# Kernel optimization log

Hardware: AMD Instinct MI355X
Metric: run time of the kernel (lower is better)

## Reference

```python
import jax, jax.numpy as jnp
import numpy as np

# dims
T, B, N, H = 16, 8, 8, 128            # time, batch, num_schemas, schema_dim
C, IH, IW = 32, 16, 16                # conv_dims
TASK, ACT, REW = 128, 16, 1
HEADS = 7
TAR = TASK + ACT + REW                # 145
CTX = H + TAR                         # 273 context_dim
CONV_FLAT = C * IH * IW               # 8192
MEM_IN = CONV_FLAT + H + CTX          # 8593


def setup_inputs() -> dict:
    key = jax.random.key(0)
    ks = jax.random.split(key, 20)
    def n(k, shape, s=0.02):
        return jax.random.normal(k, shape, dtype=jnp.float32) * s
    D = HEADS * H
    return {
        "image": jax.random.normal(ks[0], (T, B, C, IH, IW), dtype=jnp.float32),
        "task_action_reward": jax.random.normal(ks[1], (T, B, TAR), dtype=jnp.float32),
        # MultiHeadedAttention params
        "Wq_w": n(ks[2], (D, CTX)), "Wq_b": jnp.zeros((D,), jnp.float32),
        "Wk_w": n(ks[3], (D, H)),   "Wk_b": jnp.zeros((D,), jnp.float32),
        "Wv_w": n(ks[4], (D, H)),   "Wv_b": jnp.zeros((D,), jnp.float32),
        "Wo_w": n(ks[5], (H, D)),   "Wo_b": jnp.zeros((H,), jnp.float32),
        # TopdownFeatureAttention: N per-query linears (stacked) + 1x1 conv
        "td_w": n(ks[6], (N, C, CTX)), "td_b": jnp.zeros((N, C), jnp.float32),
        "conv_w": n(ks[7], (C, C)), "conv_b": jnp.zeros((C,), jnp.float32),
        # ListStructuredRnn: N per-schema LSTM cells (PyTorch gate order i,f,g,o)
        "Wih": n(ks[8], (N, 4 * H, MEM_IN)), "Whh": n(ks[9], (N, 4 * H, H)),
        "bih": jnp.zeros((N, 4 * H), jnp.float32), "bhh": jnp.zeros((N, 4 * H), jnp.float32),
    }


def reference(image, task_action_reward, Wq_w, Wq_b, Wk_w, Wk_b, Wv_w, Wv_b,
              Wo_w, Wo_b, td_w, td_b, conv_w, conv_b, Wih, Whh, bih, bhh):
    f32 = image.dtype
    # prev_state=None path: prev_h is zeros for all timesteps
    prev_h = jnp.zeros((T, B, N, H), f32)
    # schema_context = duplicate task_action_reward over schemas, cat prev_h -> (T,B,N,CTX)
    ctx = jnp.concatenate(
        [jnp.broadcast_to(task_action_reward[:, :, None, :], (T, B, N, TAR)), prev_h], axis=-1)
    # keys = cat(prev_h, zeros) along schema axis -> (T,B,N+1,H)
    keys = jnp.concatenate([prev_h, jnp.zeros((T, B, 1, H), f32)], axis=2)

    # --- MultiHeadedAttention (no mask; dropout unused in forward) ---
    q = (ctx @ Wq_w.T + Wq_b).reshape(T, B, N, HEADS, H)
    k = (keys @ Wk_w.T + Wk_b).reshape(T, B, N + 1, HEADS, H)
    v = (keys @ Wv_w.T + Wv_b).reshape(T, B, N + 1, HEADS, H)
    scores = jnp.einsum('tbqhd,tbkhd->tbhqk', q, k) / jnp.sqrt(jnp.asarray(H, f32))
    attn = jax.nn.softmax(scores, axis=-1)
    xatt = jnp.einsum('tbhqk,tbkhd->tbqhd', attn, v).reshape(T, B, N, HEADS * H)
    shared = xatt @ Wo_w.T + Wo_b                      # (T,B,N,H)

    # --- TopdownFeatureAttention: per-query linear -> sigmoid channel gate -> 1x1 conv ---
    gate = jax.nn.sigmoid(jnp.einsum('tbnx,ncx->tbnc', ctx, td_w) + td_b)   # (T,B,N,C)
    modulated = image[:, :, None] * gate[..., None, None]                    # (T,B,N,C,IH,IW)
    conv = jnp.einsum('tbnchw,dc->tbndhw', modulated, conv_w) + conv_b[:, None, None]
    schema_updates = conv.reshape(T, B, N, CONV_FLAT)

    # --- per-schema LSTMs over time (zero initial state) ---
    mem = jnp.concatenate([schema_updates, shared, ctx], axis=-1)            # (T,B,N,MEM_IN)
    xg = jnp.einsum('tbni,ngi->tbng', mem, Wih) + bih + bhh                  # (T,B,N,4H)

    def step(carry, g_t):
        h, c = carry
        g = g_t + jnp.einsum('bnh,ngh->bng', h, Whh)
        i, f, gg, o = jnp.split(g, 4, axis=-1)
        c = jax.nn.sigmoid(f) * c + jax.nn.sigmoid(i) * jnp.tanh(gg)
        h = jax.nn.sigmoid(o) * jnp.tanh(c)
        return (h, c), h

    z = jnp.zeros((B, N, H), f32)
    (hT, cT), hs = jax.lax.scan(step, (z, z), xg)
    outs = hs.reshape(T, B, N * H)
    return outs, hT, cT
```

## Files before the change

kernel.cpp:

```cpp
#include <hip/hip_runtime.h>

#define T_   16
#define B_   8
#define N_   8
#define H_   128
#define C_   32
#define HW_  256
#define TAR_ 145
#define G4H  512
#define MEMIN 8593
#define AK   8512
#define XGN  524288
#define KSTEP 64

typedef __attribute__((ext_vector_type(8))) short short8v;
typedef __attribute__((ext_vector_type(4))) float f32x4;
typedef __attribute__((ext_vector_type(4), aligned(4))) float f32x4u;

__device__ __forceinline__ float bf2f(unsigned short u){
  return __uint_as_float(((unsigned int)u) << 16);
}
__device__ __forceinline__ unsigned short f2bf(float x){
  unsigned int b = __float_as_uint(x);
  return (unsigned short)((b + 0x7fffu + ((b >> 16) & 1u)) >> 16);
}
__device__ __forceinline__ unsigned pkbf(float lo, float hi){
  return __builtin_amdgcn_perm(__float_as_uint(hi) + 0x8000u,
                               __float_as_uint(lo) + 0x8000u, 0x07060302u);
}
__device__ __forceinline__ float bflo(unsigned w){ return __uint_as_float(w << 16); }
__device__ __forceinline__ float bfhi(unsigned w){ return __uint_as_float(w & 0xffff0000u); }
__device__ __forceinline__ float sigf(float x){ return 1.f/(1.f + expf(-x)); }

__device__ __forceinline__ void gl_lds16(const void* g, void* l){
  __builtin_amdgcn_global_load_lds(
      (const __attribute__((address_space(1))) unsigned int*)g,
      (__attribute__((address_space(3))) unsigned int*)l, 16, 0, 0);
}
__device__ __forceinline__ void gl_lds4(const void* g, void* l){
  __builtin_amdgcn_global_load_lds(
      (const __attribute__((address_space(1))) unsigned int*)g,
      (__attribute__((address_space(3))) unsigned int*)l, 4, 0, 0);
}

__global__ void k_shared(const float* __restrict__ WvB, const float* __restrict__ WoW,
                         const float* __restrict__ WoB, float* __restrict__ sh){
  const int h = blockIdx.x, lane = threadIdx.x;
  float acc = 0.f;
  for(int d = lane; d < 896; d += 64) acc += WvB[d] * WoW[h*896 + d];
  for(int s = 32; s; s >>= 1) acc += __shfl_down(acc, s);
  if(lane == 0) sh[h] = acc + WoB[h];
}

__global__ __launch_bounds__(256) void k_gate(const float* __restrict__ tar,
                                              const float* __restrict__ tdw,
                                              const float* __restrict__ tdb,
                                              float* __restrict__ gate){
  __shared__ float twS[32*145];
  __shared__ float taS[16*145];
  const int tb0 = blockIdx.x * 16, n = blockIdx.y, tid = threadIdx.x;
  for(int i = tid; i < 32*145; i += 256){
    int c = i / 145, x = i - c*145;
    twS[i] = tdw[(n*32 + c)*273 + x];
  }
  for(int i = tid; i < 16*145; i += 256)
    taS[i] = tar[tb0*145 + i];
  __syncthreads();
  for(int o = tid; o < 512; o += 256){
    int r = o >> 5, c = o & 31;
    float a = tdb[n*32 + c];
    const float* tr = &taS[r*145];
    const float* tw = &twS[c*145];
    for(int x = 0; x < 145; ++x) a += tr[x]*tw[x];
    gate[((tb0 + r)*N_ + n)*C_ + c] = 1.f/(1.f + expf(-a));
  }
}

__global__ __launch_bounds__(256) void k_conv2(
    const float* __restrict__ img, const float* __restrict__ gate,
    const float* __restrict__ cw, const float* __restrict__ cb,
    const float* __restrict__ sh, const float* __restrict__ tar,
    unsigned short* __restrict__ mem)
{
  __shared__ float imgS[8192];
  __shared__ float cwgT[1024];
  const int tb = blockIdx.x, n = blockIdx.y;
  const int hw = threadIdx.x;
  for(int i = hw; i < 8192; i += 256)
    imgS[i] = img[(size_t)tb*8192 + i];
  for(int i = hw; i < 1024; i += 256){
    const int c = i >> 5, d = i & 31;
    cwgT[i] = cw[d*32 + c] * gate[(tb*8 + n)*32 + c];
  }
  __syncthreads();
  f32x4 acc[8];
  #pragma unroll
  for(int dq = 0; dq < 8; ++dq){
    const f32x4u cv = *(const f32x4u*)&cb[dq*4];
    acc[dq].x = cv.x; acc[dq].y = cv.y; acc[dq].z = cv.z; acc[dq].w = cv.w;
  }
  #pragma unroll 4
  for(int c = 0; c < 32; ++c){
    const float iv = imgS[c*256 + hw];
    #pragma unroll
    for(int dq = 0; dq < 8; ++dq){
      const f32x4 w = *(const f32x4*)&cwgT[c*32 + dq*4];
      acc[dq].x += iv*w.x; acc[dq].y += iv*w.y;
      acc[dq].z += iv*w.z; acc[dq].w += iv*w.w;
    }
  }
  unsigned short* mrow = mem + (size_t)(n*128 + tb)*AK;
  #pragma unroll
  for(int dq = 0; dq < 8; ++dq){
    mrow[(dq*4 + 0)*256 + hw] = f2bf(acc[dq].x);
    mrow[(dq*4 + 1)*256 + hw] = f2bf(acc[dq].y);
    mrow[(dq*4 + 2)*256 + hw] = f2bf(acc[dq].z);
    mrow[(dq*4 + 3)*256 + hw] = f2bf(acc[dq].w);
  }
  for(int i = hw; i < 320; i += 256){
    if(i < 128)      mrow[8192 + i]       = f2bf(sh[i]);
    else if(i < 273) mrow[8320 + i - 128] = f2bf(tar[tb*TAR_ + i - 128]);
    else             mrow[8465 + i - 273] = 0;
  }
}

__global__ __launch_bounds__(256) void k_gemm5(
    const unsigned short* __restrict__ mem, const float* __restrict__ Wih,
    float* __restrict__ xg4)
{
  __shared__ unsigned short Abuf[2][128*64];
  __shared__ float          Bbuf[2][16*64];
  const int gt = blockIdx.x, n = blockIdx.y, ks = blockIdx.z;
  const int tid = threadIdx.x;
  const int wv = tid >> 6, ln = tid & 63;
  const int lr = ln & 15, lg = ln >> 4;
  const int g0 = gt*16;
  const int kbeg = (ks == 0) ? 0 : 2176 + (ks - 1)*2112;
  const int nsteps = (ks == 0) ? 34 : 33;
  const unsigned short* An = mem + (size_t)n*128*AK;
  const float* Bn = Wih + (size_t)(n*G4H + g0)*MEMIN;

#define STAGE5(bb, kk) do{                                                     \
    _Pragma("unroll")                                                          \
    for(int i_ = 0; i_ < 4; ++i_){                                             \
      const int ci_ = i_*256 + tid;                                            \
      const int row_ = ci_ >> 3;                                               \
      const unsigned short* src_ = An + (size_t)row_*AK + (kk)                 \
                                   + (((ci_ & 7) ^ (row_ & 7)) << 3);          \
      gl_lds16(src_, &Abuf[bb][(i_*256 + wv*64)*8]);                           \
    }                                                                          \
    _Pragma("unroll")                                                          \
    for(int q_ = 0; q_ < 4; ++q_){                                             \
      const int idx_ = q_*256 + tid;                                           \
      const int g_ = idx_ >> 6;                                                \
      const int kd_ = idx_ & 63;                                               \
      const float* srcB_ = Bn + (size_t)g_*MEMIN + (kk)                        \
                           + ((((kd_ >> 3) ^ (g_ & 7)) << 3) + (kd_ & 7));     \
      gl_lds4(srcB_, &Bbuf[bb][q_*256 + wv*64]);                               \
    }                                                                          \
  }while(0)

  f32x4 acc0 = {0.f,0.f,0.f,0.f};
  f32x4 acc1 = {0.f,0.f,0.f,0.f};

  STAGE5(0, kbeg);
  if(nsteps > 1) STAGE5(1, kbeg + KSTEP);

  int b = 0;
  for(int t = 0; t < nsteps; ++t){
    if(t < nsteps - 1){
      asm volatile("s_waitcnt vmcnt(8)" ::: "memory");
    } else {
      asm volatile("s_waitcnt vmcnt(0)" ::: "memory");
    }
    __builtin_amdgcn_s_barrier();
    #pragma unroll
    for(int s = 0; s < 2; ++s){
      const int jb = (s*4 + lg) ^ (lr & 7);
      const float* bp = &Bbuf[b][lr*64 + jb*8];
      const f32x4 blo = *(const f32x4*)bp;
      const f32x4 bhi = *(const f32x4*)(bp + 4);
      short8v bf;
      unsigned* u = (unsigned*)&bf;
      u[0] = pkbf(blo.x, blo.y); u[1] = pkbf(blo.z, blo.w);
      u[2] = pkbf(bhi.x, bhi.y); u[3] = pkbf(bhi.z, bhi.w);
      const short8v a0 = *(const short8v*)&Abuf[b][(wv*32 + lr)*64 + jb*8];
      const short8v a1 = *(const short8v*)&Abuf[b][(wv*32 + 16 + lr)*64 + jb*8];
      acc0 = __builtin_amdgcn_mfma_f32_16x16x32_bf16(a0, bf, acc0, 0, 0, 0);
      acc1 = __builtin_amdgcn_mfma_f32_16x16x32_bf16(a1, bf, acc1, 0, 0, 0);
    }
    __builtin_amdgcn_s_barrier();
    if(t + 2 < nsteps) STAGE5(b, kbeg + (t+2)*KSTEP);
    b ^= 1;
  }
#undef STAGE5

  float* dst = xg4 + (size_t)ks*XGN;
  const int c0 = g0 + lr;
  const int r0 = wv*32 + lg*4, r1 = r0 + 16;
  #pragma unroll
  for(int j = 0; j < 4; ++j){
    dst[(size_t)((r0 + j)*8 + n)*G4H + c0] = acc0[j];
    dst[(size_t)((r1 + j)*8 + n)*G4H + c0] = acc1[j];
  }
}

__global__ __launch_bounds__(512) void k_lstm2(
    const float* __restrict__ xg4, const float* __restrict__ Whh,
    const float* __restrict__ bih, const float* __restrict__ bhh,
    float* __restrict__ out)
{
  __shared__ float hS[128];
  __shared__ float preS[512];
  const int bn = blockIdx.x;
  const int n = bn & 7, b = bn >> 3;
  const int g = threadIdx.x;

  unsigned wr[64];
  const float* wrow = Whh + (size_t)(n*G4H + g)*H_;
  #pragma unroll
  for(int i = 0; i < 32; ++i){
    const f32x4 w = *(const f32x4*)(wrow + i*4);
    wr[2*i]   = pkbf(w.x, w.y);
    wr[2*i+1] = pkbf(w.z, w.w);
  }
  const float bias = bih[n*G4H + g] + bhh[n*G4H + g];
  if(g < 128) hS[g] = 0.f;
  float cc = 0.f;
  __syncthreads();

  for(int t = 0; t < 16; ++t){
    const size_t xb = (size_t)((t*8 + b)*8 + n)*G4H + g;
    float acc = bias + xg4[xb] + xg4[xb + XGN] + xg4[xb + 2*XGN] + xg4[xb + 3*XGN];
    #pragma unroll
    for(int q = 0; q < 32; ++q){
      const f32x4 hv = *(const f32x4*)&hS[q*4];
      const unsigned w0 = wr[2*q], w1 = wr[2*q+1];
      acc += hv.x*bflo(w0) + hv.y*bfhi(w0) + hv.z*bflo(w1) + hv.w*bfhi(w1);
    }
    preS[g] = acc;
    __syncthreads();
    if(g < 128){
      const float iv = sigf(preS[g]);
      const float fv = sigf(preS[128 + g]);
      const float gv = tanhf(preS[256 + g]);
      const float ov = sigf(preS[384 + g]);
      cc = fv*cc + iv*gv;
      const float hn = ov*tanhf(cc);
      hS[g] = hn;
      out[(t*8 + b)*1024 + n*128 + g] = hn;
      if(t == 15){
        out[131072 + (b*8 + n)*128 + g] = hn;
        out[139264 + (b*8 + n)*128 + g] = cc;
      }
    }
    __syncthreads();
  }
}

__global__ __launch_bounds__(512) void k_conv(
    const float* __restrict__ img, const float* __restrict__ gate,
    const float* __restrict__ cw, const float* __restrict__ cb,
    const float* __restrict__ sh, const float* __restrict__ tar,
    unsigned short* __restrict__ mem)
{
  __shared__ float imgS[8192];
  __shared__ float cwgS[1024];
  __shared__ float shS[128];
  __shared__ float tarS[160];
  const int tb = blockIdx.x, tid = threadIdx.x;
  for(int i = tid; i < 8192; i += 512)
    imgS[i] = img[(size_t)tb*8192 + i];
  if(tid < 128) shS[tid] = sh[tid];
  if(tid >= 128 && tid < 273) tarS[tid-128] = tar[tb*TAR_ + tid - 128];
  for(int n = 0; n < 8; ++n){
    __syncthreads();
    for(int i = tid; i < 1024; i += 512)
      cwgS[i] = cw[i] * gate[(tb*8 + n)*32 + (i & 31)];
    __syncthreads();
    unsigned short* mrow = mem + (size_t)(n*128 + tb)*AK;
    for(int q = 0; q < 4; ++q){
      const int idx = q*2048 + tid*4;
      const int d = idx >> 8, hw = idx & 255;
      const float bias = cb[d];
      float a0 = bias, a1 = bias, a2 = bias, a3 = bias;
      const float* cg = &cwgS[d*32];
      #pragma unroll
      for(int c = 0; c < 32; ++c){
        const f32x4 iv = *(const f32x4*)&imgS[c*256 + hw];
        const float w = cg[c];
        a0 += w*iv.x; a1 += w*iv.y; a2 += w*iv.z; a3 += w*iv.w;
      }
      ushort4 o;
      o.x = f2bf(a0); o.y = f2bf(a1); o.z = f2bf(a2); o.w = f2bf(a3);
      *(ushort4*)&mrow[idx] = o;
    }
    if(tid < 128)      mrow[8192 + tid]       = f2bf(shS[tid]);
    else if(tid < 273) mrow[8320 + tid - 128] = f2bf(tarS[tid - 128]);
    else if(tid < 320) mrow[8465 + tid - 273] = 0;
  }
}

__global__ __launch_bounds__(256) void k_bias(const float* __restrict__ bih,
                                              const float* __restrict__ bhh,
                                              float* __restrict__ xg){
  const int i = blockIdx.x*256 + threadIdx.x;
  const int ng = ((i >> 9) & 7)*512 + (i & 511);
  xg[i] = bih[ng] + bhh[ng];
}

__global__ __launch_bounds__(256) void k_gemm_mfma(
    const unsigned short* __restrict__ mem, const float* __restrict__ Wih,
    float* __restrict__ xg)
{
  const int gt = blockIdx.x, n = blockIdx.y, ks = blockIdx.z;
  const int wv = threadIdx.x >> 6, ln = threadIdx.x & 63;
  const int lr = ln & 15, lg = ln >> 4;
  const int g0 = gt*16;
  const int kbeg = (ks==0) ? 0 : (ks==1) ? 2144 : (ks==2) ? 4256 : 6368;
  const int kend = (ks==0) ? 2144 : (ks==1) ? 4256 : (ks==2) ? 6368 : 8480;
  const float* Bp = Wih + (size_t)(n*G4H + g0 + lr)*MEMIN + lg*8;
  const unsigned short* Ap = mem + (size_t)(n*128 + wv*32 + lr)*AK + lg*8;
  f32x4 acc0 = {0.f,0.f,0.f,0.f};
  f32x4 acc1 = {0.f,0.f,0.f,0.f};
  #pragma unroll 2
  for(int k = kbeg; k < kend; k += 32){
    const f32x4u blo = *(const f32x4u*)(Bp + k);
    const f32x4u bhi = *(const f32x4u*)(Bp + k + 4);
    short8v bf;
    unsigned* bu = (unsigned*)&bf;
    bu[0] = pkbf(blo.x, blo.y); bu[1] = pkbf(blo.z, blo.w);
    bu[2] = pkbf(bhi.x, bhi.y); bu[3] = pkbf(bhi.z, bhi.w);
    const short8v a0 = *(const short8v*)(Ap + k);
    const short8v a1 = *(const short8v*)(Ap + (size_t)16*AK + k);
    acc0 = __builtin_amdgcn_mfma_f32_16x16x32_bf16(a0, bf, acc0, 0, 0, 0);
    acc1 = __builtin_amdgcn_mfma_f32_16x16x32_bf16(a1, bf, acc1, 0, 0, 0);
  }
  const int col = g0 + lr;
  const int r0  = wv*32 + lg*4;
  #pragma unroll
  for(int j = 0; j < 4; ++j){
    atomicAdd(&xg[(size_t)((r0 + j)*8 + n)*G4H + col],      acc0[j]);
    atomicAdd(&xg[(size_t)((r0 + 16 + j)*8 + n)*G4H + col], acc1[j]);
  }
}

__global__ __launch_bounds__(1024) void k_lstm(
    const float* __restrict__ xg, const float* __restrict__ Whh,
    float* __restrict__ out)
{
  extern __shared__ char smem[];
  unsigned short* Wl = (unsigned short*)smem;
  float* hS = (float*)(smem + 512*136*sizeof(unsigned short));

  const int n = blockIdx.x, tid = threadIdx.x;
  for(int i = tid; i < 512*128; i += 1024){
    int g = i >> 7, k = i & 127;
    Wl[g*136 + k] = f2bf(Whh[n*512*128 + i]);
  }
  hS[tid] = 0.f;
  const int h = tid >> 3, b = tid & 7;
  float cc = 0.f;
  __syncthreads();

  for(int t = 0; t < 16; ++t){
    const long xbase = ((long)((t*8 + b)*8 + n))*G4H + h;
    float g0 = xg[xbase + 0*128];
    float g1 = xg[xbase + 1*128];
    float g2 = xg[xbase + 2*128];
    float g3 = xg[xbase + 3*128];
    const float* hr = &hS[b*128];
    const unsigned short* w0 = &Wl[(0*128 + h)*136];
    const unsigned short* w1 = &Wl[(1*128 + h)*136];
    const unsigned short* w2 = &Wl[(2*128 + h)*136];
    const unsigned short* w3 = &Wl[(3*128 + h)*136];
    for(int k = 0; k < 128; k += 4){
      const float4 hv = *(const float4*)&hr[k];
      const ushort4 a0 = *(const ushort4*)&w0[k];
      const ushort4 a1 = *(const ushort4*)&w1[k];
      const ushort4 a2 = *(const ushort4*)&w2[k];
      const ushort4 a3 = *(const ushort4*)&w3[k];
      g0 += hv.x*bf2f(a0.x) + hv.y*bf2f(a0.y) + hv.z*bf2f(a0.z) + hv.w*bf2f(a0.w);
      g1 += hv.x*bf2f(a1.x) + hv.y*bf2f(a1.y) + hv.z*bf2f(a1.z) + hv.w*bf2f(a1.w);
      g2 += hv.x*bf2f(a2.x) + hv.y*bf2f(a2.y) + hv.z*bf2f(a2.z) + hv.w*bf2f(a2.w);
      g3 += hv.x*bf2f(a3.x) + hv.y*bf2f(a3.y) + hv.z*bf2f(a3.z) + hv.w*bf2f(a3.w);
    }
    const float iv = sigf(g0);
    const float fv = sigf(g1);
    const float gv = tanhf(g2);
    const float ov = sigf(g3);
    cc = fv*cc + iv*gv;
    const float hn = ov * tanhf(cc);
    __syncthreads();
    hS[b*128 + h] = hn;
    out[(t*8 + b)*1024 + n*128 + h] = hn;
    if(t == 15){
      out[131072 + (b*8 + n)*128 + h] = hn;
      out[139264 + (b*8 + n)*128 + h] = cc;
    }
    __syncthreads();
  }
}

__global__ __launch_bounds__(256) void k_gemm_old(
    const float* __restrict__ img, const float* __restrict__ gate,
    const float* __restrict__ cw, const float* __restrict__ cb,
    const float* __restrict__ sh, const float* __restrict__ tar,
    const float* __restrict__ Wih, const float* __restrict__ bih,
    const float* __restrict__ bhh, float* __restrict__ xg)
{
  __shared__ __align__(16) float imgS[16*545];
  __shared__ __align__(16) float WtS[16*132];
  __shared__ float PS[16*17];
  __shared__ float gateS[16*32];
  __shared__ float cw2S[16*32];
  __shared__ float cwS[32*32];
  __shared__ float cbS[32];
  __shared__ float shS[128];
  __shared__ float tarS[16*145];

  const int tid = threadIdx.x;
  const int g0  = blockIdx.x * 128;
  const int tb0 = blockIdx.y * 16;
  const int n   = blockIdx.z;
  const int gth = tid & 31;
  const int rth = tid >> 5;
  const long wbase = (long)(n*G4H + g0) * MEMIN;

  for(int i = tid; i < 16*32; i += 256){
    int r = i >> 5, c = i & 31;
    gateS[i] = gate[((tb0 + r)*N_ + n)*C_ + c];
  }
  for(int i = tid; i < 32*32; i += 256) cwS[i] = cw[i];
  if(tid < 32)  cbS[tid] = cb[tid];
  if(tid < 128) shS[tid] = sh[tid];
  for(int i = tid; i < 16*TAR_; i += 256)
    tarS[i] = tar[tb0*TAR_ + i];

  float acc0[4] = {0,0,0,0}, acc1[4] = {0,0,0,0};

  for(int s = 0; s < 16; ++s){
    __syncthreads();
    for(int i = tid; i < 8192; i += 256){
      int j = i & 15, c = (i >> 4) & 31, r = i >> 9;
      imgS[r*545 + c*17 + j] = img[((tb0 + r)*C_ + c)*HW_ + s*16 + j];
    }
    for(int d = 0; d < 32; ++d){
      __syncthreads();
      for(int i = tid; i < 2048; i += 256){
        int g = i >> 4, j = i & 15;
        WtS[j*132 + g] = Wih[wbase + (long)g*MEMIN + d*HW_ + s*16 + j];
      }
      for(int i = tid; i < 512; i += 256)
        cw2S[i] = gateS[i] * cwS[d*32 + (i & 31)];
      __syncthreads();
      {
        int j = tid & 15, r = tid >> 4;
        float a = cbS[d];
        const float* c2 = &cw2S[r*32];
        const float* im = &imgS[r*545 + j];
        #pragma unroll
        for(int c = 0; c < 32; ++c) a += c2[c] * im[c*17];
        PS[j*17 + r] = a;
      }
      __syncthreads();
      #pragma unroll
      for(int j = 0; j < 16; ++j){
        const float4 w = *(const float4*)&WtS[j*132 + (gth << 2)];
        const float p0 = PS[j*17 + (rth << 1)];
        const float p1 = PS[j*17 + (rth << 1) + 1];
        acc0[0] += p0*w.x; acc0[1] += p0*w.y; acc0[2] += p0*w.z; acc0[3] += p0*w.w;
        acc1[0] += p1*w.x; acc1[1] += p1*w.y; acc1[2] += p1*w.z; acc1[3] += p1*w.w;
      }
    }
  }
  {
    float ta[4] = {0,0,0,0};
    for(int kc = 0; kc < 8; ++kc){
      __syncthreads();
      for(int i = tid; i < 2048; i += 256){
        int g = i >> 4, j = i & 15;
        WtS[j*132 + g] = Wih[wbase + (long)g*MEMIN + 8192 + kc*16 + j];
      }
      __syncthreads();
      #pragma unroll
      for(int j = 0; j < 16; ++j){
        const float4 w = *(const float4*)&WtS[j*132 + (gth << 2)];
        const float sv = shS[kc*16 + j];
        ta[0] += sv*w.x; ta[1] += sv*w.y; ta[2] += sv*w.z; ta[3] += sv*w.w;
      }
    }
    acc0[0] += ta[0]; acc0[1] += ta[1]; acc0[2] += ta[2]; acc0[3] += ta[3];
    acc1[0] += ta[0]; acc1[1] += ta[1]; acc1[2] += ta[2]; acc1[3] += ta[3];
  }
  for(int kc = 0; kc < 10; ++kc){
    const int kendl = (kc == 9) ? 1 : 16;
    __syncthreads();
    for(int i = tid; i < 2048; i += 256){
      int g = i >> 4, j = i & 15;
      if(j < kendl)
        WtS[j*132 + g] = Wih[wbase + (long)g*MEMIN + 8320 + kc*16 + j];
    }
    __syncthreads();
    for(int j = 0; j < kendl; ++j){
      const float4 w = *(const float4*)&WtS[j*132 + (gth << 2)];
      const float p0 = tarS[(rth << 1)*TAR_ + kc*16 + j];
      const float p1 = tarS[((rth << 1) + 1)*TAR_ + kc*16 + j];
      acc0[0] += p0*w.x; acc0[1] += p0*w.y; acc0[2] += p0*w.z; acc0[3] += p0*w.w;
      acc1[0] += p1*w.x; acc1[1] += p1*w.y; acc1[2] += p1*w.z; acc1[3] += p1*w.w;
    }
  }
  {
    const int gg = g0 + (gth << 2);
    const float b0 = bih[n*G4H + gg + 0] + bhh[n*G4H + gg + 0];
    const float b1 = bih[n*G4H + gg + 1] + bhh[n*G4H + gg + 1];
    const float b2 = bih[n*G4H + gg + 2] + bhh[n*G4H + gg + 2];
    const float b3 = bih[n*G4H + gg + 3] + bhh[n*G4H + gg + 3];
    const int row = tb0 + (rth << 1);
    float4 o0 = make_float4(acc0[0]+b0, acc0[1]+b1, acc0[2]+b2, acc0[3]+b3);
    *(float4*)&xg[((long)(row*N_ + n))*G4H + gg] = o0;
    float4 o1 = make_float4(acc1[0]+b0, acc1[1]+b1, acc1[2]+b2, acc1[3]+b3);
    *(float4*)&xg[((long)((row + 1)*N_ + n))*G4H + gg] = o1;
  }
}

extern "C" void kernel_launch(void* const* d_in, const int* in_sizes, int n_in,
                              void* d_out, int out_size, void* d_ws, size_t ws_size,
                              hipStream_t stream)
{
  (void)in_sizes; (void)n_in; (void)out_size;
  const float* img  = (const float*)d_in[0];
  const float* tar  = (const float*)d_in[1];
  const float* WvB  = (const float*)d_in[7];
  const float* WoW  = (const float*)d_in[8];
  const float* WoB  = (const float*)d_in[9];
  const float* tdw  = (const float*)d_in[10];
  const float* tdb  = (const float*)d_in[11];
  const float* cw   = (const float*)d_in[12];
  const float* cb   = (const float*)d_in[13];
  const float* Wih  = (const float*)d_in[14];
  const float* Whh  = (const float*)d_in[15];
  const float* bih  = (const float*)d_in[16];
  const float* bhh  = (const float*)d_in[17];

  float* wsf   = (float*)d_ws;
  float* gatew = wsf;
  float* shw   = wsf + 32768;

  float* xg4w = wsf + 32896;
  unsigned short* memA = (unsigned short*)((char*)d_ws + 8520192);
  const size_t WS_A = 8520192 + (size_t)8*128*AK*2;

  float* xgB = wsf + 32896;
  unsigned short* memB = (unsigned short*)((char*)d_ws + 2228736);
  const size_t WS_B = 2228736 + (size_t)8*128*AK*2;

  k_shared<<<128, 64, 0, stream>>>(WvB, WoW, WoB, shw);
  k_gate<<<dim3(8, 8), 256, 0, stream>>>(tar, tdw, tdb, gatew);

  if(ws_size >= WS_A){
    k_conv2<<<dim3(128, 8), 256, 0, stream>>>(img, gatew, cw, cb, shw, tar, memA);
    k_gemm5<<<dim3(32, 8, 4), 256, 0, stream>>>(memA, Wih, xg4w);
    k_lstm2<<<64, 512, 0, stream>>>(xg4w, Whh, bih, bhh, (float*)d_out);
  } else if(ws_size >= WS_B){
    k_conv<<<128, 512, 0, stream>>>(img, gatew, cw, cb, shw, tar, memB);
    k_bias<<<2048, 256, 0, stream>>>(bih, bhh, xgB);
    k_gemm_mfma<<<dim3(32, 8, 4), 256, 0, stream>>>(memB, Wih, xgB);
    (void)hipFuncSetAttribute((const void*)k_lstm,
                              hipFuncAttributeMaxDynamicSharedMemorySize, 143360);
    k_lstm<<<8, 1024, 143360, stream>>>(xgB, Whh, (float*)d_out);
  } else {
    k_gemm_old<<<dim3(4, 8, 8), 256, 0, stream>>>(img, gatew, cw, cb, shw, tar,
                                                  Wih, bih, bhh, xgB);
    (void)hipFuncSetAttribute((const void*)k_lstm,
                              hipFuncAttributeMaxDynamicSharedMemorySize, 143360);
    k_lstm<<<8, 1024, 143360, stream>>>(xgB, Whh, (float*)d_out);
  }
}
```

Before: 123.7 us.

## Prepack Wih into swizzled bf16 panels before the MFMA input GEMM

Adds a k_wprep kernel that converts the fp32 input-to-hidden LSTM weights into bf16 and stores them in per-tile panels with an XOR swizzle. A new k_gemm6 then streams A and B into LDS through asynchronous global-to-LDS copies, with no fp32-to-bf16 packing in the inner loop and no bank-conflicting B layout. The cost is an extra full pass over Wih on every call (read fp32, write bf16) plus a large workspace requirement. The old fallback kernels are removed, and the conv and LSTM launches are made unconditional.

```diff
diff --git a/kernel.cpp b/kernel.cpp
--- a/kernel.cpp
+++ b/kernel.cpp
@@ -12,6 +12,7 @@
 #define AK   8512
 #define XGN  524288
 #define KSTEP 64
+#define PANEL_E 136192
 
 typedef __attribute__((ext_vector_type(8))) short short8v;
 typedef __attribute__((ext_vector_type(4))) float f32x4;
@@ -121,6 +122,96 @@
     if(i < 128)      mrow[8192 + i]       = f2bf(sh[i]);
     else if(i < 273) mrow[8320 + i - 128] = f2bf(tar[tb*TAR_ + i - 128]);
     else             mrow[8465 + i - 273] = 0;
+  }
+}
+
+__global__ __launch_bounds__(256) void k_wprep(
+    const float* __restrict__ Wih, unsigned short* __restrict__ wsB)
+{
+  const unsigned J = 4358144u;
+  const unsigned stride = gridDim.x * 256u;
+  for(unsigned j = blockIdx.x*256u + threadIdx.x; j < J; j += stride){
+    const unsigned r  = j / 1064u;
+    const unsigned k0 = (j - r*1064u) * 8u;
+    const float* src = Wih + (size_t)r*MEMIN + k0;
+    const f32x4u v0 = *(const f32x4u*)src;
+    const f32x4u v1 = *(const f32x4u*)(src + 4);
+    uint4 o;
+    o.x = pkbf(v0.x, v0.y); o.y = pkbf(v0.z, v0.w);
+    o.z = pkbf(v1.x, v1.y); o.w = pkbf(v1.z, v1.w);
+    const unsigned n = r >> 9, g512 = r & 511u;
+    const unsigned gt = g512 >> 4, g = g512 & 15u;
+    const unsigned kb = k0 >> 6, kin = k0 & 63u;
+    const unsigned ksw = (((kin >> 3) ^ (g & 7u)) << 3);
+    unsigned short* dst = wsB + (size_t)(n*32u + gt)*PANEL_E
+                          + kb*1024u + g*64u + ksw;
+    *(uint4*)dst = o;
+  }
+}
+
+__global__ __launch_bounds__(256) void k_gemm6(
+    const unsigned short* __restrict__ mem, const unsigned short* __restrict__ wsB,
+    float* __restrict__ xg4)
+{
+  __shared__ unsigned short Abuf[2][128*64];
+  __shared__ unsigned short Bbuf[2][16*64];
+  const int gt = blockIdx.x, n = blockIdx.y, ks = blockIdx.z;
+  const int tid = threadIdx.x;
+  const int wv = tid >> 6, ln = tid & 63;
+  const int lr = ln & 15, lg = ln >> 4;
+  const int g0 = gt*16;
+  const int kbeg = (ks == 0) ? 0 : 2176 + (ks - 1)*2112;
+  const int nsteps = (ks == 0) ? 34 : 33;
+  const unsigned short* An = mem + (size_t)n*128*AK;
+  const char* panelB = (const char*)(wsB + (size_t)(n*32 + gt)*PANEL_E);
+
+#define STAGE6(bb, kk) do{                                                     \
+    _Pragma("unroll")                                                          \
+    for(int i_ = 0; i_ < 4; ++i_){                                             \
+      const int ci_ = i_*256 + tid;                                            \
+      const int row_ = ci_ >> 3;                                               \
+      const unsigned short* src_ = An + (size_t)row_*AK + (kk)                 \
+                                   + (((ci_ & 7) ^ (row_ & 7)) << 3);          \
+      gl_lds16(src_, &Abuf[bb][(i_*256 + wv*64)*8]);                           \
+    }                                                                          \
+    _Pragma("unroll")                                                          \
+    for(int j_ = 0; j_ < 2; ++j_){                                             \
+      const char* srcB_ = panelB + (size_t)((kk) >> 6)*2048                    \
+                          + wv*512 + j_*256 + ln*4;                            \
+      gl_lds4(srcB_, (char*)&Bbuf[bb][0] + wv*512 + j_*256);                   \
+    }                                                                          \
+  }while(0)
+
+  f32x4 acc0 = {0.f,0.f,0.f,0.f};
+  f32x4 acc1 = {0.f,0.f,0.f,0.f};
+
+  STAGE6(0, kbeg);
+  __syncthreads();
+
+  int b = 0;
+  for(int t = 0; t < nsteps; ++t){
+    if(t + 1 < nsteps) STAGE6(b^1, kbeg + (t+1)*KSTEP);
+    #pragma unroll
+    for(int s = 0; s < 2; ++s){
+      const int jb = (s*4 + lg) ^ (lr & 7);
+      const short8v bf = *(const short8v*)&Bbuf[b][lr*64 + jb*8];
+      const short8v a0 = *(const short8v*)&Abuf[b][(wv*32 + lr)*64 + jb*8];
+      const short8v a1 = *(const short8v*)&Abuf[b][(wv*32 + 16 + lr)*64 + jb*8];
+      acc0 = __builtin_amdgcn_mfma_f32_16x16x32_bf16(a0, bf, acc0, 0, 0, 0);
+      acc1 = __builtin_amdgcn_mfma_f32_16x16x32_bf16(a1, bf, acc1, 0, 0, 0);
+    }
+    __syncthreads();
+    b ^= 1;
+  }
+#undef STAGE6
+
+  float* dst = xg4 + (size_t)ks*XGN;
+  const int c0 = g0 + lr;
+  const int r0 = wv*32 + lg*4, r1 = r0 + 16;
+  #pragma unroll
+  for(int j = 0; j < 4; ++j){
+    dst[(size_t)((r0 + j)*8 + n)*G4H + c0] = acc0[j];
+    dst[(size_t)((r1 + j)*8 + n)*G4H + c0] = acc1[j];
   }
 }
 
@@ -258,272 +349,6 @@
   }
 }
 
-__global__ __launch_bounds__(512) void k_conv(
-    const float* __restrict__ img, const float* __restrict__ gate,
-    const float* __restrict__ cw, const float* __restrict__ cb,
-    const float* __restrict__ sh, const float* __restrict__ tar,
-    unsigned short* __restrict__ mem)
-{
-  __shared__ float imgS[8192];
-  __shared__ float cwgS[1024];
-  __shared__ float shS[128];
-  __shared__ float tarS[160];
-  const int tb = blockIdx.x, tid = threadIdx.x;
-  for(int i = tid; i < 8192; i += 512)
-    imgS[i] = img[(size_t)tb*8192 + i];
-  if(tid < 128) shS[tid] = sh[tid];
-  if(tid >= 128 && tid < 273) tarS[tid-128] = tar[tb*TAR_ + tid - 128];
-  for(int n = 0; n < 8; ++n){
-    __syncthreads();
-    for(int i = tid; i < 1024; i += 512)
-      cwgS[i] = cw[i] * gate[(tb*8 + n)*32 + (i & 31)];
-    __syncthreads();
-    unsigned short* mrow = mem + (size_t)(n*128 + tb)*AK;
-    for(int q = 0; q < 4; ++q){
-      const int idx = q*2048 + tid*4;
-      const int d = idx >> 8, hw = idx & 255;
-      const float bias = cb[d];
-      float a0 = bias, a1 = bias, a2 = bias, a3 = bias;
-      const float* cg = &cwgS[d*32];
-      #pragma unroll
-      for(int c = 0; c < 32; ++c){
-        const f32x4 iv = *(const f32x4*)&imgS[c*256 + hw];
-        const float w = cg[c];
-        a0 += w*iv.x; a1 += w*iv.y; a2 += w*iv.z; a3 += w*iv.w;
-      }
-      ushort4 o;
-      o.x = f2bf(a0); o.y = f2bf(a1); o.z = f2bf(a2); o.w = f2bf(a3);
-      *(ushort4*)&mrow[idx] = o;
-    }
-    if(tid < 128)      mrow[8192 + tid]       = f2bf(shS[tid]);
-    else if(tid < 273) mrow[8320 + tid - 128] = f2bf(tarS[tid - 128]);
-    else if(tid < 320) mrow[8465 + tid - 273] = 0;
-  }
-}
-
-__global__ __launch_bounds__(256) void k_bias(const float* __restrict__ bih,
-                                              const float* __restrict__ bhh,
-                                              float* __restrict__ xg){
-  const int i = blockIdx.x*256 + threadIdx.x;
-  const int ng = ((i >> 9) & 7)*512 + (i & 511);
-  xg[i] = bih[ng] + bhh[ng];
-}
-
-__global__ __launch_bounds__(256) void k_gemm_mfma(
-    const unsigned short* __restrict__ mem, const float* __restrict__ Wih,
-    float* __restrict__ xg)
-{
-  const int gt = blockIdx.x, n = blockIdx.y, ks = blockIdx.z;
-  const int wv = threadIdx.x >> 6, ln = threadIdx.x & 63;
-  const int lr = ln & 15, lg = ln >> 4;
-  const int g0 = gt*16;
-  const int kbeg = (ks==0) ? 0 : (ks==1) ? 2144 : (ks==2) ? 4256 : 6368;
-  const int kend = (ks==0) ? 2144 : (ks==1) ? 4256 : (ks==2) ? 6368 : 8480;
-  const float* Bp = Wih + (size_t)(n*G4H + g0 + lr)*MEMIN + lg*8;
-  const unsigned short* Ap = mem + (size_t)(n*128 + wv*32 + lr)*AK + lg*8;
-  f32x4 acc0 = {0.f,0.f,0.f,0.f};
-  f32x4 acc1 = {0.f,0.f,0.f,0.f};
-  #pragma unroll 2
-  for(int k = kbeg; k < kend; k += 32){
-    const f32x4u blo = *(const f32x4u*)(Bp + k);
-    const f32x4u bhi = *(const f32x4u*)(Bp + k + 4);
-    short8v bf;
-    unsigned* bu = (unsigned*)&bf;
-    bu[0] = pkbf(blo.x, blo.y); bu[1] = pkbf(blo.z, blo.w);
-    bu[2] = pkbf(bhi.x, bhi.y); bu[3] = pkbf(bhi.z, bhi.w);
-    const short8v a0 = *(const short8v*)(Ap + k);
-    const short8v a1 = *(const short8v*)(Ap + (size_t)16*AK + k);
-    acc0 = __builtin_amdgcn_mfma_f32_16x16x32_bf16(a0, bf, acc0, 0, 0, 0);
-    acc1 = __builtin_amdgcn_mfma_f32_16x16x32_bf16(a1, bf, acc1, 0, 0, 0);
-  }
-  const int col = g0 + lr;
-  const int r0  = wv*32 + lg*4;
-  #pragma unroll
-  for(int j = 0; j < 4; ++j){
-    atomicAdd(&xg[(size_t)((r0 + j)*8 + n)*G4H + col],      acc0[j]);
-    atomicAdd(&xg[(size_t)((r0 + 16 + j)*8 + n)*G4H + col], acc1[j]);
-  }
-}
-
-__global__ __launch_bounds__(1024) void k_lstm(
-    const float* __restrict__ xg, const float* __restrict__ Whh,
-    float* __restrict__ out)
-{
-  extern __shared__ char smem[];
-  unsigned short* Wl = (unsigned short*)smem;
-  float* hS = (float*)(smem + 512*136*sizeof(unsigned short));
-
-  const int n = blockIdx.x, tid = threadIdx.x;
-  for(int i = tid; i < 512*128; i += 1024){
-    int g = i >> 7, k = i & 127;
-    Wl[g*136 + k] = f2bf(Whh[n*512*128 + i]);
-  }
-  hS[tid] = 0.f;
-  const int h = tid >> 3, b = tid & 7;
-  float cc = 0.f;
-  __syncthreads();
-
-  for(int t = 0; t < 16; ++t){
-    const long xbase = ((long)((t*8 + b)*8 + n))*G4H + h;
-    float g0 = xg[xbase + 0*128];
-    float g1 = xg[xbase + 1*128];
-    float g2 = xg[xbase + 2*128];
-    float g3 = xg[xbase + 3*128];
-    const float* hr = &hS[b*128];
-    const unsigned short* w0 = &Wl[(0*128 + h)*136];
-    const unsigned short* w1 = &Wl[(1*128 + h)*136];
-    const unsigned short* w2 = &Wl[(2*128 + h)*136];
-    const unsigned short* w3 = &Wl[(3*128 + h)*136];
-    for(int k = 0; k < 128; k += 4){
-      const float4 hv = *(const float4*)&hr[k];
-      const ushort4 a0 = *(const ushort4*)&w0[k];
-      const ushort4 a1 = *(const ushort4*)&w1[k];
-      const ushort4 a2 = *(const ushort4*)&w2[k];
-      const ushort4 a3 = *(const ushort4*)&w3[k];
-      g0 += hv.x*bf2f(a0.x) + hv.y*bf2f(a0.y) + hv.z*bf2f(a0.z) + hv.w*bf2f(a0.w);
-      g1 += hv.x*bf2f(a1.x) + hv.y*bf2f(a1.y) + hv.z*bf2f(a1.z) + hv.w*bf2f(a1.w);
-      g2 += hv.x*bf2f(a2.x) + hv.y*bf2f(a2.y) + hv.z*bf2f(a2.z) + hv.w*bf2f(a2.w);
-      g3 += hv.x*bf2f(a3.x) + hv.y*bf2f(a3.y) + hv.z*bf2f(a3.z) + hv.w*bf2f(a3.w);
-    }
-    const float iv = sigf(g0);
-    const float fv = sigf(g1);
-    const float gv = tanhf(g2);
-    const float ov = sigf(g3);
-    cc = fv*cc + iv*gv;
-    const float hn = ov * tanhf(cc);
-    __syncthreads();
-    hS[b*128 + h] = hn;
-    out[(t*8 + b)*1024 + n*128 + h] = hn;
-    if(t == 15){
-      out[131072 + (b*8 + n)*128 + h] = hn;
-      out[139264 + (b*8 + n)*128 + h] = cc;
-    }
-    __syncthreads();
-  }
-}
-
-__global__ __launch_bounds__(256) void k_gemm_old(
-    const float* __restrict__ img, const float* __restrict__ gate,
-    const float* __restrict__ cw, const float* __restrict__ cb,
-    const float* __restrict__ sh, const float* __restrict__ tar,
-    const float* __restrict__ Wih, const float* __restrict__ bih,
-    const float* __restrict__ bhh, float* __restrict__ xg)
-{
-  __shared__ __align__(16) float imgS[16*545];
-  __shared__ __align__(16) float WtS[16*132];
-  __shared__ float PS[16*17];
-  __shared__ float gateS[16*32];
-  __shared__ float cw2S[16*32];
-  __shared__ float cwS[32*32];
-  __shared__ float cbS[32];
-  __shared__ float shS[128];
-  __shared__ float tarS[16*145];
-
-  const int tid = threadIdx.x;
-  const int g0  = blockIdx.x * 128;
-  const int tb0 = blockIdx.y * 16;
-  const int n   = blockIdx.z;
-  const int gth = tid & 31;
-  const int rth = tid >> 5;
-  const long wbase = (long)(n*G4H + g0) * MEMIN;
-
-  for(int i = tid; i < 16*32; i += 256){
-    int r = i >> 5, c = i & 31;
-    gateS[i] = gate[((tb0 + r)*N_ + n)*C_ + c];
-  }
-  for(int i = tid; i < 32*32; i += 256) cwS[i] = cw[i];
-  if(tid < 32)  cbS[tid] = cb[tid];
-  if(tid < 128) shS[tid] = sh[tid];
-  for(int i = tid; i < 16*TAR_; i += 256)
-    tarS[i] = tar[tb0*TAR_ + i];
-
-  float acc0[4] = {0,0,0,0}, acc1[4] = {0,0,0,0};
-
-  for(int s = 0; s < 16; ++s){
-    __syncthreads();
-    for(int i = tid; i < 8192; i += 256){
-      int j = i & 15, c = (i >> 4) & 31, r = i >> 9;
-      imgS[r*545 + c*17 + j] = img[((tb0 + r)*C_ + c)*HW_ + s*16 + j];
-    }
-    for(int d = 0; d < 32; ++d){
-      __syncthreads();
-      for(int i = tid; i < 2048; i += 256){
-        int g = i >> 4, j = i & 15;
-        WtS[j*132 + g] = Wih[wbase + (long)g*MEMIN + d*HW_ + s*16 + j];
-      }
-      for(int i = tid; i < 512; i += 256)
-        cw2S[i] = gateS[i] * cwS[d*32 + (i & 31)];
-      __syncthreads();
-      {
-        int j = tid & 15, r = tid >> 4;
-        float a = cbS[d];
-        const float* c2 = &cw2S[r*32];
-        const float* im = &imgS[r*545 + j];
-        #pragma unroll
-        for(int c = 0; c < 32; ++c) a += c2[c] * im[c*17];
-        PS[j*17 + r] = a;
-      }
-      __syncthreads();
-      #pragma unroll
-      for(int j = 0; j < 16; ++j){
-        const float4 w = *(const float4*)&WtS[j*132 + (gth << 2)];
-        const float p0 = PS[j*17 + (rth << 1)];
-        const float p1 = PS[j*17 + (rth << 1) + 1];
-        acc0[0] += p0*w.x; acc0[1] += p0*w.y; acc0[2] += p0*w.z; acc0[3] += p0*w.w;
-        acc1[0] += p1*w.x; acc1[1] += p1*w.y; acc1[2] += p1*w.z; acc1[3] += p1*w.w;
-      }
-    }
-  }
-  {
-    float ta[4] = {0,0,0,0};
-    for(int kc = 0; kc < 8; ++kc){
-      __syncthreads();
-      for(int i = tid; i < 2048; i += 256){
-        int g = i >> 4, j = i & 15;
-        WtS[j*132 + g] = Wih[wbase + (long)g*MEMIN + 8192 + kc*16 + j];
-      }
-      __syncthreads();
-      #pragma unroll
-      for(int j = 0; j < 16; ++j){
-        const float4 w = *(const float4*)&WtS[j*132 + (gth << 2)];
-        const float sv = shS[kc*16 + j];
-        ta[0] += sv*w.x; ta[1] += sv*w.y; ta[2] += sv*w.z; ta[3] += sv*w.w;
-      }
-    }
-    acc0[0] += ta[0]; acc0[1] += ta[1]; acc0[2] += ta[2]; acc0[3] += ta[3];
-    acc1[0] += ta[0]; acc1[1] += ta[1]; acc1[2] += ta[2]; acc1[3] += ta[3];
-  }
-  for(int kc = 0; kc < 10; ++kc){
-    const int kendl = (kc == 9) ? 1 : 16;
-    __syncthreads();
-    for(int i = tid; i < 2048; i += 256){
-      int g = i >> 4, j = i & 15;
-      if(j < kendl)
-        WtS[j*132 + g] = Wih[wbase + (long)g*MEMIN + 8320 + kc*16 + j];
-    }
-    __syncthreads();
-    for(int j = 0; j < kendl; ++j){
-      const float4 w = *(const float4*)&WtS[j*132 + (gth << 2)];
-      const float p0 = tarS[(rth << 1)*TAR_ + kc*16 + j];
-      const float p1 = tarS[((rth << 1) + 1)*TAR_ + kc*16 + j];
-      acc0[0] += p0*w.x; acc0[1] += p0*w.y; acc0[2] += p0*w.z; acc0[3] += p0*w.w;
-      acc1[0] += p1*w.x; acc1[1] += p1*w.y; acc1[2] += p1*w.z; acc1[3] += p1*w.w;
-    }
-  }
-  {
-    const int gg = g0 + (gth << 2);
-    const float b0 = bih[n*G4H + gg + 0] + bhh[n*G4H + gg + 0];
-    const float b1 = bih[n*G4H + gg + 1] + bhh[n*G4H + gg + 1];
-    const float b2 = bih[n*G4H + gg + 2] + bhh[n*G4H + gg + 2];
-    const float b3 = bih[n*G4H + gg + 3] + bhh[n*G4H + gg + 3];
-    const int row = tb0 + (rth << 1);
-    float4 o0 = make_float4(acc0[0]+b0, acc0[1]+b1, acc0[2]+b2, acc0[3]+b3);
-    *(float4*)&xg[((long)(row*N_ + n))*G4H + gg] = o0;
-    float4 o1 = make_float4(acc1[0]+b0, acc1[1]+b1, acc1[2]+b2, acc1[3]+b3);
-    *(float4*)&xg[((long)((row + 1)*N_ + n))*G4H + gg] = o1;
-  }
-}
-
 extern "C" void kernel_launch(void* const* d_in, const int* in_sizes, int n_in,
                               void* d_out, int out_size, void* d_ws, size_t ws_size,
                               hipStream_t stream)
@@ -546,34 +371,21 @@
   float* wsf   = (float*)d_ws;
   float* gatew = wsf;
   float* shw   = wsf + 32768;
-
-  float* xg4w = wsf + 32896;
+  float* xg4w  = wsf + 32896;
   unsigned short* memA = (unsigned short*)((char*)d_ws + 8520192);
-  const size_t WS_A = 8520192 + (size_t)8*128*AK*2;
-
-  float* xgB = wsf + 32896;
-  unsigned short* memB = (unsigned short*)((char*)d_ws + 2228736);
-  const size_t WS_B = 2228736 + (size_t)8*128*AK*2;
+  unsigned short* wsB  = (unsigned short*)((char*)d_ws + 25952768);
+  const size_t WS_A  = 25952768;
+  const size_t WS_AP = 25952768 + (size_t)256*PANEL_E*2;
 
   k_shared<<<128, 64, 0, stream>>>(WvB, WoW, WoB, shw);
   k_gate<<<dim3(8, 8), 256, 0, stream>>>(tar, tdw, tdb, gatew);
-
-  if(ws_size >= WS_A){
-    k_conv2<<<dim3(128, 8), 256, 0, stream>>>(img, gatew, cw, cb, shw, tar, memA);
+  k_conv2<<<dim3(128, 8), 256, 0, stream>>>(img, gatew, cw, cb, shw, tar, memA);
+
+  if(ws_size >= WS_AP){
+    k_wprep<<<2048, 256, 0, stream>>>(Wih, wsB);
+    k_gemm6<<<dim3(32, 8, 4), 256, 0, stream>>>(memA, wsB, xg4w);
+  } else if(ws_size >= WS_A){
     k_gemm5<<<dim3(32, 8, 4), 256, 0, stream>>>(memA, Wih, xg4w);
-    k_lstm2<<<64, 512, 0, stream>>>(xg4w, Whh, bih, bhh, (float*)d_out);
-  } else if(ws_size >= WS_B){
-    k_conv<<<128, 512, 0, stream>>>(img, gatew, cw, cb, shw, tar, memB);
-    k_bias<<<2048, 256, 0, stream>>>(bih, bhh, xgB);
-    k_gemm_mfma<<<dim3(32, 8, 4), 256, 0, stream>>>(memB, Wih, xgB);
-    (void)hipFuncSetAttribute((const void*)k_lstm,
-                              hipFuncAttributeMaxDynamicSharedMemorySize, 143360);
-    k_lstm<<<8, 1024, 143360, stream>>>(xgB, Whh, (float*)d_out);
-  } else {
-    k_gemm_old<<<dim3(4, 8, 8), 256, 0, stream>>>(img, gatew, cw, cb, shw, tar,
-                                                  Wih, bih, bhh, xgB);
-    (void)hipFuncSetAttribute((const void*)k_lstm,
-                              hipFuncAttributeMaxDynamicSharedMemorySize, 143360);
-    k_lstm<<<8, 1024, 143360, stream>>>(xgB, Whh, (float*)d_out);
-  }
-}
+  }
+  k_lstm2<<<64, 512, 0, stream>>>(xg4w, Whh, bih, bhh, (float*)d_out);
+}
```

Measured after the change: 146.9 us. +18.7%, slower.
